# Kernel tuning notes

Hardware: AMD Instinct MI355X
Metric: run time of the kernel (lower is better)

## Reference

```python
import jax, jax.numpy as jnp
import numpy as np

H, CH, INF, EPS = 16, 24, 1e9, 1e-5

def layer_norm(x, w, b):
    mu = jnp.mean(x, axis=-1, keepdims=True)
    var = jnp.mean(jnp.square(x - mu), axis=-1, keepdims=True)
    return (x - mu) * jax.lax.rsqrt(var + EPS) * w + b

def setup_inputs() -> dict:
    key = jax.random.key(0)
    ks = jax.random.split(key, 10)
    B, N, C, CZ = 1, 768, 384, 128
    sc = 0.02
    return {
        "a": jax.random.normal(ks[0], (B, N, C), jnp.float32),
        "z": jax.random.normal(ks[1], (B, N, N, CZ), jnp.float32),
        "mask": jnp.ones((B, N), jnp.float32),
        "ln_a_w": jnp.ones((C,), jnp.float32),
        "ln_a_b": jnp.zeros((C,), jnp.float32),
        "ln_z_w": jnp.ones((CZ,), jnp.float32),
        "ln_z_b": jnp.zeros((CZ,), jnp.float32),
        "Wz": jax.random.normal(ks[2], (CZ, H), jnp.float32) * sc,
        "Wq": jax.random.normal(ks[3], (C, H * CH), jnp.float32) * sc,
        "Wk": jax.random.normal(ks[4], (C, H * CH), jnp.float32) * sc,
        "Wv": jax.random.normal(ks[5], (C, H * CH), jnp.float32) * sc,
        "Wg": jax.random.normal(ks[6], (C, H * CH), jnp.float32) * sc,
        "bg": jnp.ones((H * CH,), jnp.float32),
        "Wo": jax.random.normal(ks[7], (H * CH, C), jnp.float32) * sc,
        "bo": jnp.zeros((C,), jnp.float32),
    }

def reference(a, z, mask, ln_a_w, ln_a_b, ln_z_w, ln_z_b, Wz, Wq, Wk, Wv, Wg, bg, Wo, bo):
    B, N, C = a.shape
    an = layer_norm(a, ln_a_w, ln_a_b)                          # [B,N,C]
    # bias terms
    mask_bias = (INF * (mask - 1.0))[:, None, None, :]          # [B,1,1,N]
    pair_bias = jnp.einsum('bijc,ch->bhij', layer_norm(z, ln_z_w, ln_z_b), Wz)  # [B,H,N,N]
    # attention
    q = (an @ Wq).reshape(B, N, H, CH) * (CH ** -0.5)
    k = (an @ Wk).reshape(B, N, H, CH)
    v = (an @ Wv).reshape(B, N, H, CH)
    scores = jnp.einsum('bqhc,bkhc->bhqk', q, k) + mask_bias + pair_bias
    p = jax.nn.softmax(scores, axis=-1)
    o = jnp.einsum('bhqk,bkhc->bqhc', p, v).reshape(B, N, H * CH)
    g = jax.nn.sigmoid(an @ Wg + bg)                            # gating from query data
    return (g * o) @ Wo + bo                                    # [B,N,C]
```

## Files before the change

kernel.cpp:

```cpp
#include <hip/hip_runtime.h>
#include <math.h>

#define NT 768
#define CD 384
#define CZD 128
#define NH 16
#define CHD 24
#define HCD 384

__global__ __launch_bounds__(64) void k_prep(
    const float* __restrict__ a, const float* __restrict__ law, const float* __restrict__ lab,
    const float* __restrict__ lzw, const float* __restrict__ lzb, const float* __restrict__ Wz,
    float* __restrict__ an, float* __restrict__ Wp, float* __restrict__ PQ)
{
    const int b = blockIdx.x;
    const int lane = threadIdx.x;
    if (b < NT) {
        const float* row = a + b * CD;
        float v[6]; float s = 0.f, sq = 0.f;
        #pragma unroll
        for (int k = 0; k < 6; ++k) { float x = row[lane + 64*k]; v[k] = x; s += x; sq += x*x; }
        #pragma unroll
        for (int off = 32; off >= 1; off >>= 1) { s += __shfl_xor(s, off); sq += __shfl_xor(sq, off); }
        const float mu = s * (1.f/CD);
        const float rs = rsqrtf(sq * (1.f/CD) - mu*mu + 1e-5f);
        #pragma unroll
        for (int k = 0; k < 6; ++k) {
            int c = lane + 64*k;
            an[b*CD + c] = (v[k] - mu) * rs * law[c] + lab[c];
        }
    } else {
        for (int idx = lane; idx < CZD*NH; idx += 64)
            Wp[idx] = lzw[idx >> 4] * Wz[idx];
        if (lane < NH) {
            float P = 0.f, Q = 0.f;
            for (int c = 0; c < CZD; ++c) {
                P += lzw[c] * Wz[c*NH + lane];
                Q += lzb[c] * Wz[c*NH + lane];
            }
            PQ[lane] = P; PQ[NH + lane] = Q;
        }
    }
}

__global__ __launch_bounds__(128) void k_proj(
    const float* __restrict__ an, const float* __restrict__ Wq, const float* __restrict__ Wk,
    const float* __restrict__ Wv, const float* __restrict__ Wg, const float* __restrict__ bg,
    float* __restrict__ qm, float* __restrict__ kT, float* __restrict__ vT, float* __restrict__ gm)
{
    __shared__ __align__(16) float Atf[16*36];
    __shared__ __align__(16) float Btf[16*68];
    const int ct = blockIdx.x;
    const int mat = ct / 6;
    const int n0 = (ct % 6) * 64;
    const int i0 = blockIdx.y * 32;
    const float* __restrict__ W = (mat == 0) ? Wq : (mat == 1) ? Wk : (mat == 2) ? Wv : Wg;
    const int t = threadIdx.x;
    const int tr = t >> 4, tc = t & 15;
    float acc[4][4] = {};
    const int kkA = t & 15, iA = t >> 4;
    const int kkB = t >> 6, nB = t & 63;
    for (int k0 = 0; k0 < CD; k0 += 16) {
        __syncthreads();
        #pragma unroll
        for (int s = 0; s < 4; ++s)
            Atf[kkA*36 + iA + 8*s] = an[(i0 + iA + 8*s)*CD + k0 + kkA];
        #pragma unroll
        for (int s = 0; s < 8; ++s)
            Btf[(kkB + 2*s)*68 + nB] = W[(k0 + kkB + 2*s)*HCD + n0 + nB];
        __syncthreads();
        #pragma unroll
        for (int kk = 0; kk < 16; ++kk) {
            const float4 a4 = *(const float4*)&Atf[kk*36 + tr*4];
            const float4 b4 = *(const float4*)&Btf[kk*68 + tc*4];
            acc[0][0] += a4.x*b4.x; acc[0][1] += a4.x*b4.y; acc[0][2] += a4.x*b4.z; acc[0][3] += a4.x*b4.w;
            acc[1][0] += a4.y*b4.x; acc[1][1] += a4.y*b4.y; acc[1][2] += a4.y*b4.z; acc[1][3] += a4.y*b4.w;
            acc[2][0] += a4.z*b4.x; acc[2][1] += a4.z*b4.y; acc[2][2] += a4.z*b4.z; acc[2][3] += a4.z*b4.w;
            acc[3][0] += a4.w*b4.x; acc[3][1] += a4.w*b4.y; acc[3][2] += a4.w*b4.z; acc[3][3] += a4.w*b4.w;
        }
    }
    #pragma unroll
    for (int r = 0; r < 4; ++r) {
        const int i = i0 + tr*4 + r;
        #pragma unroll
        for (int c = 0; c < 4; ++c) {
            const int n = n0 + tc*4 + c;
            const float v = acc[r][c];
            if (mat == 0)      qm[i*HCD + n] = v * 0.20412414523193154f;
            else if (mat == 1) kT[n*NT + i] = v;
            else if (mat == 2) vT[n*NT + i] = v;
            else               gm[i*HCD + n] = 1.f / (1.f + __expf(-(v + bg[n])));
        }
    }
}

__global__ __launch_bounds__(256) void k_bias(
    const float* __restrict__ z, const float* __restrict__ Wp, const float* __restrict__ PQ,
    float* __restrict__ bias)
{
    const int t = threadIdx.x;
    const size_t r = (size_t)blockIdx.x * 256 + t;
    const float4* __restrict__ zr = (const float4*)(z + r * CZD);
    const float4* __restrict__ Wp4 = (const float4*)Wp;
    float s = 0.f, q = 0.f;
    float acc[16] = {};
    #pragma unroll 8
    for (int c4 = 0; c4 < 32; ++c4) {
        const float4 v = zr[c4];
        const float xs[4] = {v.x, v.y, v.z, v.w};
        #pragma unroll
        for (int e = 0; e < 4; ++e) {
            const float x = xs[e];
            s += x; q += x*x;
            const int c = c4*4 + e;
            const float4 w0 = Wp4[c*4+0], w1 = Wp4[c*4+1], w2 = Wp4[c*4+2], w3 = Wp4[c*4+3];
            acc[0]+=x*w0.x;  acc[1]+=x*w0.y;  acc[2]+=x*w0.z;  acc[3]+=x*w0.w;
            acc[4]+=x*w1.x;  acc[5]+=x*w1.y;  acc[6]+=x*w1.z;  acc[7]+=x*w1.w;
            acc[8]+=x*w2.x;  acc[9]+=x*w2.y;  acc[10]+=x*w2.z; acc[11]+=x*w2.w;
            acc[12]+=x*w3.x; acc[13]+=x*w3.y; acc[14]+=x*w3.z; acc[15]+=x*w3.w;
        }
    }
    const float mu = s * (1.f/CZD);
    const float rs = rsqrtf(q * (1.f/CZD) - mu*mu + 1e-5f);
    #pragma unroll
    for (int h = 0; h < 16; ++h)
        bias[(size_t)h*NT*NT + r] = rs*(acc[h] - mu*PQ[h]) + PQ[16+h];
}

__global__ __launch_bounds__(256) void k_attn(
    const float* __restrict__ qm, const float* __restrict__ kT, const float* __restrict__ vT,
    const float* __restrict__ bias, const float* __restrict__ mask, float* __restrict__ om)
{
    __shared__ __align__(16) char smem[17408];
    float (*ks)[68] = (float(*)[68])smem;
    float (*vs)[28] = (float(*)[28])(smem + 6528);
    float (*qs)[25] = (float(*)[25])(smem + 13696);
    float* mb       = (float*)(smem + 16896);
    float (*po)[32][25] = (float(*)[32][25])smem;
    float* pmf      = (float*)(smem + 12800);
    float* plf      = (float*)(smem + 13312);

    const int h  = blockIdx.x;
    const int i0 = blockIdx.y * 32;
    const int t = threadIdx.x;
    const int lane = t & 63, wave = t >> 6;
    const int i2 = lane & 31;
    const int jg8 = ((wave << 1) + (lane >> 5)) * 8;

    for (int idx = t; idx < 32*CHD; idx += 256) {
        const int ii = idx / CHD, c = idx % CHD;
        qs[ii][c] = qm[(i0+ii)*HCD + h*CHD + c];
    }
    __syncthreads();
    float qr[24];
    #pragma unroll
    for (int c = 0; c < 24; ++c) qr[c] = qs[i2][c];
    float m_ = -1e30f, l_ = 0.f;
    float ov[24] = {};

    for (int jt = 0; jt < NT; jt += 64) {
        __syncthreads();
        for (int idx = t; idx < 24*64; idx += 256) {
            const int c = idx >> 6, j = idx & 63;
            ks[c][j] = kT[(h*CHD + c)*NT + jt + j];
            vs[j][c] = vT[(h*CHD + c)*NT + jt + j];
        }
        if (t < 64) mb[t] = 1e9f * (mask[jt + t] - 1.f);
        __syncthreads();

        const float* bp = bias + ((size_t)h*NT + (size_t)(i0 + i2))*NT + jt + jg8;
        const float4 b0 = *(const float4*)bp;
        const float4 b1 = *(const float4*)(bp + 4);
        float sc[8] = {b0.x, b0.y, b0.z, b0.w, b1.x, b1.y, b1.z, b1.w};
        #pragma unroll
        for (int jj = 0; jj < 8; ++jj) sc[jj] += mb[jg8+jj];
        #pragma unroll
        for (int c = 0; c < 24; ++c) {
            const float4 k4a = *(const float4*)&ks[c][jg8];
            const float4 k4b = *(const float4*)&ks[c][jg8+4];
            const float q0 = qr[c];
            sc[0] += q0*k4a.x; sc[1] += q0*k4a.y; sc[2] += q0*k4a.z; sc[3] += q0*k4a.w;
            sc[4] += q0*k4b.x; sc[5] += q0*k4b.y; sc[6] += q0*k4b.z; sc[7] += q0*k4b.w;
        }
        float mt = sc[0];
        #pragma unroll
        for (int jj = 1; jj < 8; ++jj) mt = fmaxf(mt, sc[jj]);
        const float mn = fmaxf(m_, mt);
        const float al = __expf(m_ - mn);
        m_ = mn;
        float p[8], ps = 0.f;
        #pragma unroll
        for (int jj = 0; jj < 8; ++jj) { p[jj] = __expf(sc[jj] - mn); ps += p[jj]; }
        l_ = l_*al + ps;
        #pragma unroll
        for (int c = 0; c < 24; ++c) ov[c] *= al;
        #pragma unroll
        for (int jj = 0; jj < 8; ++jj) {
            #pragma unroll
            for (int c4 = 0; c4 < 6; ++c4) {
                const float4 v4 = *(const float4*)&vs[jg8+jj][c4*4];
                ov[c4*4+0] += p[jj]*v4.x; ov[c4*4+1] += p[jj]*v4.y;
                ov[c4*4+2] += p[jj]*v4.z; ov[c4*4+3] += p[jj]*v4.w;
            }
        }
    }
    {
        const float mo = __shfl_xor(m_, 32);
        const float lo = __shfl_xor(l_, 32);
        const float mn = fmaxf(m_, mo);
        const float wa = __expf(m_ - mn), wb = __expf(mo - mn);
        l_ = l_*wa + lo*wb;
        m_ = mn;
        #pragma unroll
        for (int c = 0; c < 24; ++c)
            ov[c] = ov[c]*wa + __shfl_xor(ov[c], 32)*wb;
    }
    __syncthreads();
    if (lane < 32) {
        pmf[wave*32 + i2] = m_; plf[wave*32 + i2] = l_;
        #pragma unroll
        for (int c = 0; c < 24; ++c) po[wave][i2][c] = ov[c];
    }
    __syncthreads();
    {
        const int i = t & 31, cq = t >> 5;
        float ms = -1e30f;
        #pragma unroll
        for (int g = 0; g < 4; ++g) ms = fmaxf(ms, pmf[g*32 + i]);
        float ls = 0.f, o0 = 0.f, o1 = 0.f, o2 = 0.f;
        #pragma unroll
        for (int g = 0; g < 4; ++g) {
            const float w = __expf(pmf[g*32 + i] - ms);
            ls += w * plf[g*32 + i];
            o0 += w * po[g][i][cq*3+0];
            o1 += w * po[g][i][cq*3+1];
            o2 += w * po[g][i][cq*3+2];
        }
        const float inv = 1.f / ls;
        float* dst = om + (size_t)(i0 + i)*HCD + h*CHD + cq*3;
        dst[0] = o0*inv; dst[1] = o1*inv; dst[2] = o2*inv;
    }
}

__global__ __launch_bounds__(128) void k_epi(
    const float* __restrict__ gm, const float* __restrict__ om, const float* __restrict__ Wo,
    const float* __restrict__ bo, float* __restrict__ out)
{
    __shared__ __align__(16) float Atf[16*36];
    __shared__ __align__(16) float Btf[16*68];
    const int n0 = blockIdx.x * 64;
    const int i0 = blockIdx.y * 32;
    const int t = threadIdx.x;
    const int tr = t >> 4, tc = t & 15;
    float acc[4][4] = {};
    const int kkA = t & 15, iA = t >> 4;
    const int kkB = t >> 6, nB = t & 63;
    for (int k0 = 0; k0 < HCD; k0 += 16) {
        __syncthreads();
        #pragma unroll
        for (int s = 0; s < 4; ++s) {
            const int row = i0 + iA + 8*s;
            Atf[kkA*36 + iA + 8*s] = gm[row*HCD + k0 + kkA] * om[row*HCD + k0 + kkA];
        }
        #pragma unroll
        for (int s = 0; s < 8; ++s)
            Btf[(kkB + 2*s)*68 + nB] = Wo[(k0 + kkB + 2*s)*CD + n0 + nB];
        __syncthreads();
        #pragma unroll
        for (int kk = 0; kk < 16; ++kk) {
            const float4 a4 = *(const float4*)&Atf[kk*36 + tr*4];
            const float4 b4 = *(const float4*)&Btf[kk*68 + tc*4];
            acc[0][0] += a4.x*b4.x; acc[0][1] += a4.x*b4.y; acc[0][2] += a4.x*b4.z; acc[0][3] += a4.x*b4.w;
            acc[1][0] += a4.y*b4.x; acc[1][1] += a4.y*b4.y; acc[1][2] += a4.y*b4.z; acc[1][3] += a4.y*b4.w;
            acc[2][0] += a4.z*b4.x; acc[2][1] += a4.z*b4.y; acc[2][2] += a4.z*b4.z; acc[2][3] += a4.z*b4.w;
            acc[3][0] += a4.w*b4.x; acc[3][1] += a4.w*b4.y; acc[3][2] += a4.w*b4.z; acc[3][3] += a4.w*b4.w;
        }
    }
    #pragma unroll
    for (int r = 0; r < 4; ++r) {
        const int i = i0 + tr*4 + r;
        #pragma unroll
        for (int c = 0; c < 4; ++c) {
            const int n = n0 + tc*4 + c;
            out[i*CD + n] = acc[r][c] + bo[n];
        }
    }
}

extern "C" void kernel_launch(void* const* d_in, const int* in_sizes, int n_in,
                              void* d_out, int out_size, void* d_ws, size_t ws_size,
                              hipStream_t stream) {
    const float* a    = (const float*)d_in[0];
    const float* z    = (const float*)d_in[1];
    const float* mask = (const float*)d_in[2];
    const float* law  = (const float*)d_in[3];
    const float* lab  = (const float*)d_in[4];
    const float* lzw  = (const float*)d_in[5];
    const float* lzb  = (const float*)d_in[6];
    const float* Wz   = (const float*)d_in[7];
    const float* Wq   = (const float*)d_in[8];
    const float* Wk   = (const float*)d_in[9];
    const float* Wv   = (const float*)d_in[10];
    const float* Wg   = (const float*)d_in[11];
    const float* bg   = (const float*)d_in[12];
    const float* Wo   = (const float*)d_in[13];
    const float* bo   = (const float*)d_in[14];
    float* out = (float*)d_out;

    float* ws = (float*)d_ws;
    float* an   = ws;
    float* qm   = an + 294912;
    float* kT   = qm + 294912;
    float* vT   = kT + 294912;
    float* gm   = vT + 294912;
    float* om   = gm + 294912;
    float* Wp   = om + 294912;
    float* PQ   = Wp + 2048;
    float* bias = PQ + 32;

    k_prep<<<769, 64, 0, stream>>>(a, law, lab, lzw, lzb, Wz, an, Wp, PQ);
    k_proj<<<dim3(24, 24), 128, 0, stream>>>(an, Wq, Wk, Wv, Wg, bg, qm, kT, vT, gm);
    k_bias<<<2304, 256, 0, stream>>>(z, Wp, PQ, bias);
    k_attn<<<dim3(16, 24), 256, 0, stream>>>(qm, kT, vT, bias, mask, om);
    k_epi<<<dim3(6, 24), 128, 0, stream>>>(gm, om, Wo, bo, out);
}
```

Baseline: 567.5 us.

## Stage z rows through shared memory with coalesced loads and split channels across four threads

The pair-bias kernel now loads 64 z rows per block into padded shared memory with fully coalesced float4 reads, instead of each thread reading its own 512-byte row with strided accesses. Four threads now share each row, each covering 32 channels, and their partial sums are combined with xor shuffles. Each thread then writes 4 of the 16 head outputs. The grid grows fourfold, which adds LDS traffic, a barrier and shuffle reductions per block in exchange for better global-load coalescing on the 300MB z read.

```diff
diff --git a/kernel.cpp b/kernel.cpp
--- a/kernel.cpp
+++ b/kernel.cpp
@@ -98,21 +98,32 @@
     const float* __restrict__ z, const float* __restrict__ Wp, const float* __restrict__ PQ,
     float* __restrict__ bias)
 {
+    __shared__ float zt[64*132];
     const int t = threadIdx.x;
-    const size_t r = (size_t)blockIdx.x * 256 + t;
-    const float4* __restrict__ zr = (const float4*)(z + r * CZD);
+    const size_t r0 = (size_t)blockIdx.x * 64;
+    const float4* __restrict__ zsrc = (const float4*)(z + r0 * CZD);
+    #pragma unroll
+    for (int it = 0; it < 8; ++it) {
+        const int f4 = t + 256*it;
+        const int row = f4 >> 5, c4 = f4 & 31;
+        const float4 v = zsrc[f4];
+        *(float4*)&zt[row*132 + c4*4] = v;
+    }
+    __syncthreads();
+    const int row = t >> 2, qd = t & 3;
+    const float* zr = &zt[row*132 + qd*32];
     const float4* __restrict__ Wp4 = (const float4*)Wp;
     float s = 0.f, q = 0.f;
     float acc[16] = {};
-    #pragma unroll 8
-    for (int c4 = 0; c4 < 32; ++c4) {
-        const float4 v = zr[c4];
+    #pragma unroll
+    for (int e = 0; e < 8; ++e) {
+        const float4 v = *(const float4*)&zr[e*4];
         const float xs[4] = {v.x, v.y, v.z, v.w};
         #pragma unroll
-        for (int e = 0; e < 4; ++e) {
-            const float x = xs[e];
+        for (int u = 0; u < 4; ++u) {
+            const float x = xs[u];
             s += x; q += x*x;
-            const int c = c4*4 + e;
+            const int c = qd*32 + e*4 + u;
             const float4 w0 = Wp4[c*4+0], w1 = Wp4[c*4+1], w2 = Wp4[c*4+2], w3 = Wp4[c*4+3];
             acc[0]+=x*w0.x;  acc[1]+=x*w0.y;  acc[2]+=x*w0.z;  acc[3]+=x*w0.w;
             acc[4]+=x*w1.x;  acc[5]+=x*w1.y;  acc[6]+=x*w1.z;  acc[7]+=x*w1.w;
@@ -120,11 +131,20 @@
             acc[12]+=x*w3.x; acc[13]+=x*w3.y; acc[14]+=x*w3.z; acc[15]+=x*w3.w;
         }
     }
+    #pragma unroll
+    for (int off = 1; off <= 2; off <<= 1) {
+        s += __shfl_xor(s, off); q += __shfl_xor(q, off);
+        #pragma unroll
+        for (int h = 0; h < 16; ++h) acc[h] += __shfl_xor(acc[h], off);
+    }
+    const size_t r = r0 + row;
     const float mu = s * (1.f/CZD);
     const float rs = rsqrtf(q * (1.f/CZD) - mu*mu + 1e-5f);
     #pragma unroll
-    for (int h = 0; h < 16; ++h)
+    for (int u = 0; u < 4; ++u) {
+        const int h = qd*4 + u;
         bias[(size_t)h*NT*NT + r] = rs*(acc[h] - mu*PQ[h]) + PQ[16+h];
+    }
 }
 
 __global__ __launch_bounds__(256) void k_attn(
@@ -320,7 +340,7 @@
 
     k_prep<<<769, 64, 0, stream>>>(a, law, lab, lzw, lzb, Wz, an, Wp, PQ);
     k_proj<<<dim3(24, 24), 128, 0, stream>>>(an, Wq, Wk, Wv, Wg, bg, qm, kT, vT, gm);
-    k_bias<<<2304, 256, 0, stream>>>(z, Wp, PQ, bias);
+    k_bias<<<9216, 256, 0, stream>>>(z, Wp, PQ, bias);
     k_attn<<<dim3(16, 24), 256, 0, stream>>>(qm, kT, vT, bias, mask, om);
     k_epi<<<dim3(6, 24), 128, 0, stream>>>(gm, om, Wo, bo, out);
 }
```

Measured after the change: 1.001 ms. +76.3%, slower.
